# Optimization experiments

Hardware: AMD Instinct MI355X
Metric: run time of the kernel (lower is better)

The kernel has to match this reference:

```python
import jax, jax.numpy as jnp
import numpy as np

DIM, NH, HD = 1536, 12, 128
F, H, W = 1, 30, 52
SEQ = F * H * W          # 1560 tokens per AR group
NG, GI = 6, 5            # num_groups, group_idx (attend over full prefix)
POS, EPS = 1024, 1e-6


def _rope_table():
    # cos/sin table matching Wan rope_params: bands [c-2(c//3), c//3, c//3] of head_dim//2
    c = HD // 2
    parts = [c - 2 * (c // 3), c // 3, c // 3]
    pos = np.arange(POS, dtype=np.float64)
    angs = []
    for cp in parts:
        inv = 1.0 / (10000.0 ** (np.arange(cp, dtype=np.float64) / cp))
        angs.append(pos[:, None] * inv[None, :])
    ang = np.concatenate(angs, axis=1)  # [POS, c]
    return jnp.asarray(np.stack([np.cos(ang), np.sin(ang)], axis=-1), dtype=jnp.float32)


def setup_inputs() -> dict:
    key = jax.random.key(0)
    ks = jax.random.split(key, 8)
    lin = lambda k: jax.random.normal(k, (DIM, DIM), jnp.float32) * 0.02
    total = NG * SEQ
    return {
        'x': jax.random.normal(ks[0], (1, SEQ, DIM), jnp.float32),
        'wq': lin(ks[1]), 'bq': jnp.zeros((DIM,), jnp.float32),
        'wk': lin(ks[2]), 'bk': jnp.zeros((DIM,), jnp.float32),
        'wv': lin(ks[3]), 'bv': jnp.zeros((DIM,), jnp.float32),
        'wo': lin(ks[4]), 'bo': jnp.zeros((DIM,), jnp.float32),
        'nq_w': jnp.ones((DIM,), jnp.float32),
        'nk_w': jnp.ones((DIM,), jnp.float32),
        'freqs': _rope_table(),
        'k_cache': jax.random.normal(ks[5], (1, total, NH, HD), jnp.float32) * 0.5,
        'v_cache': jax.random.normal(ks[6], (1, total, NH, HD), jnp.float32) * 0.5,
        'f': F, 'h': H, 'w': W, 'group_idx': GI, 'num_groups': NG,
    }


def _rms_norm(x, weight, eps=EPS):
    # fast_rms_norm: normalize over the full channel dim, then scale
    x = x.astype(jnp.float32)
    return x * jax.lax.rsqrt(jnp.mean(x * x, axis=-1, keepdims=True) + eps) * weight


def _rope_apply(x, freqs, f, h, w, group_idx):
    # x: [B, S, N, D] with S = f*h*w; freqs: [POS, D//2, 2] (cos, sin)
    B, S, N, D = x.shape
    c = D // 2
    cf = c - 2 * (c // 3)
    ch = cw = c // 3
    sf = group_idx * f
    fp = jnp.broadcast_to(freqs[sf:sf + f, :cf][:, None, None], (f, h, w, cf, 2))
    hp = jnp.broadcast_to(freqs[:h, cf:cf + ch][None, :, None], (f, h, w, ch, 2))
    wp = jnp.broadcast_to(freqs[:w, cf + ch:][None, None, :], (f, h, w, cw, 2))
    rot = jnp.concatenate([fp, hp, wp], axis=3).reshape(S, c, 2)  # [S, c, 2]
    cos = rot[..., 0][None, :, None]  # [1, S, 1, c]
    sin = rot[..., 1][None, :, None]
    xr = x.astype(jnp.float32).reshape(B, S, N, c, 2)
    out_r = xr[..., 0] * cos - xr[..., 1] * sin  # complex multiply x * e^{i theta}
    out_i = xr[..., 0] * sin + xr[..., 1] * cos
    return jnp.stack([out_r, out_i], axis=-1).reshape(B, S, N, D)


def reference(x, wq, bq, wk, bk, wv, bv, wo, bo, nq_w, nk_w, freqs,
              k_cache, v_cache, f, h, w, group_idx, num_groups):
    B, S, C = x.shape
    n, d = NH, C // NH
    q = _rms_norm(x @ wq.T + bq, nq_w).reshape(B, S, n, d)
    k = _rms_norm(x @ wk.T + bk, nk_w).reshape(B, S, n, d)
    v = (x @ wv.T + bv).reshape(B, S, n, d)
    q = _rope_apply(q, freqs, f, h, w, group_idx)
    k = _rope_apply(k, freqs, f, h, w, group_idx)
    # KV-cache scatter (detached in the original) then prefix gather
    start = group_idx * S
    kc = jax.lax.dynamic_update_slice(k_cache, jax.lax.stop_gradient(k), (0, start, 0, 0))
    vc = jax.lax.dynamic_update_slice(v_cache, jax.lax.stop_gradient(v), (0, start, 0, 0))
    k_full = kc[:, :start + S]  # [B, Lkv, n, d]
    v_full = vc[:, :start + S]
    att = jnp.einsum('bqnd,bknd->bnqk', q, k_full) / jnp.sqrt(jnp.float32(d))
    p = jax.nn.softmax(att, axis=-1)
    o = jnp.einsum('bnqk,bknd->bqnd', p, v_full).reshape(B, S, C)
    return o @ wo.T + bo
```

## Files before the change

### kernel.cpp

```cpp
#include <hip/hip_runtime.h>

#define DIM 1536
#define NH 12
#define HD 128
#define KSPLIT 8
#define KT 32
#define MFIX 3.0f
#define KK48 48

typedef _Float16 half2_t __attribute__((ext_vector_type(2)));
typedef _Float16 half8_t __attribute__((ext_vector_type(8)));
typedef float f32x4 __attribute__((ext_vector_type(4)));

__device__ __forceinline__ half2_t pkrtz(float a, float b) {
    return __builtin_bit_cast(half2_t, __builtin_amdgcn_cvt_pkrtz(a, b));
}

__device__ __forceinline__ void split8(float4 a, float4 b, half8_t& h, half8_t& l) {
    half2_t h0 = pkrtz(a.x, a.y), h1 = pkrtz(a.z, a.w);
    half2_t h2 = pkrtz(b.x, b.y), h3 = pkrtz(b.z, b.w);
    half2_t g0 = pkrtz(a.x - (float)h0.x, a.y - (float)h0.y);
    half2_t g1 = pkrtz(a.z - (float)h1.x, a.w - (float)h1.y);
    half2_t g2 = pkrtz(b.x - (float)h2.x, b.y - (float)h2.y);
    half2_t g3 = pkrtz(b.z - (float)h3.x, b.w - (float)h3.y);
    h[0]=h0.x; h[1]=h0.y; h[2]=h1.x; h[3]=h1.y; h[4]=h2.x; h[5]=h2.y; h[6]=h3.x; h[7]=h3.y;
    l[0]=g0.x; l[1]=g0.y; l[2]=g1.x; l[3]=g1.y; l[4]=g2.x; l[5]=g2.y; l[6]=g3.x; l[7]=g3.y;
}

__device__ __forceinline__ half8_t cvt8rn(float4 a, float4 b) {
    half8_t h;
    h[0]=(_Float16)a.x; h[1]=(_Float16)a.y; h[2]=(_Float16)a.z; h[3]=(_Float16)a.w;
    h[4]=(_Float16)b.x; h[5]=(_Float16)b.y; h[6]=(_Float16)b.z; h[7]=(_Float16)b.w;
    return h;
}

__device__ __forceinline__ void gl2lds16(const void* g, void* l) {
    __builtin_amdgcn_global_load_lds(
        (const __attribute__((address_space(1))) unsigned int*)g,
        (__attribute__((address_space(3))) unsigned int*)(unsigned int)(uintptr_t)l,
        16, 0, 0);
}


__global__ __launch_bounds__(256) void cvt_a_fl(
    const float* __restrict__ src, _Float16* __restrict__ h, _Float16* __restrict__ l,
    int M, int nrec8)
{
    const int i = blockIdx.x * 256 + threadIdx.x;
    if (i >= nrec8) return;
    const int lane = i & 63;
    const int grp  = (i >> 6) & 7;
    const int tile = i >> 9;
    const int kk = tile % KK48, mt = tile / KK48;
    const int row = mt * 128 + grp * 16 + (lane & 15);
    const int k   = kk * 32 + (lane >> 4) * 8;
    float4 a = make_float4(0,0,0,0), b = a;
    if (row < M) {
        const float* s = src + (size_t)row * DIM + k;
        a = *(const float4*)s; b = *(const float4*)(s + 4);
    }
    half8_t hh, ll; split8(a, b, hh, ll);
    ((half8_t*)h)[i] = hh;
    ((half8_t*)l)[i] = ll;
}

__global__ __launch_bounds__(256) void cvt_w_fl(
    const float* __restrict__ s0, const float* __restrict__ s1,
    const float* __restrict__ s2, const float* __restrict__ s3,
    _Float16* __restrict__ h0, _Float16* __restrict__ l0,
    _Float16* __restrict__ h1, _Float16* __restrict__ l1,
    _Float16* __restrict__ h2, _Float16* __restrict__ l2,
    _Float16* __restrict__ h3, _Float16* __restrict__ l3, int nrec8)
{
    const int i = blockIdx.x * 256 + threadIdx.x;
    if (i >= nrec8) return;
    const int m = blockIdx.y;
    const float* src = m == 0 ? s0 : m == 1 ? s1 : m == 2 ? s2 : s3;
    _Float16* h = m == 0 ? h0 : m == 1 ? h1 : m == 2 ? h2 : h3;
    _Float16* l = m == 0 ? l0 : m == 1 ? l1 : m == 2 ? l2 : l3;
    const int lane = i & 63;
    const int grp  = (i >> 6) & 7;
    const int tile = i >> 9;
    const int kk = tile % KK48, nt = tile / KK48;
    const int row = nt * 128 + grp * 16 + (lane & 15);
    const int k   = kk * 32 + (lane >> 4) * 8;
    const float* s = src + (size_t)row * DIM + k;
    float4 a = *(const float4*)s, b = *(const float4*)(s + 4);
    half8_t hh, ll; split8(a, b, hh, ll);
    ((half8_t*)h)[i] = hh;
    if (m >= 2) ((half8_t*)l)[i] = ll;
}

__global__ __launch_bounds__(256, 4) void gemm_fl_s(
    const _Float16* __restrict__ Ah,
    const _Float16* __restrict__ Bh0, const _Float16* __restrict__ Bh1,
    const float* __restrict__ bias0, const float* __restrict__ bias1,
    float* __restrict__ C0, float* __restrict__ C1,
    int M)
{
    __shared__ __align__(16) _Float16 T[2][2][4096];

    const int nwg = gridDim.x;
    const int L = blockIdx.x;
    const int q8 = nwg >> 3, r8 = nwg & 7;
    const int xcd = L & 7, si = L >> 3;
    const int logical = (xcd < r8 ? xcd * (q8 + 1)
                                  : r8 * (q8 + 1) + (xcd - r8) * q8) + si;
    const int j   = logical % 24;
    const int myy = logical / 24;
    const int mat = j & 1, nt = j >> 1;
    const _Float16* Bh   = mat ? Bh1 : Bh0;
    const float*    bias = mat ? bias1 : bias0;
    float*          C    = mat ? C1 : C0;
    const int m0 = myy * 128, n0 = nt * 128;

    const int tid = threadIdx.x;
    const int lane = tid & 63, wave = tid >> 6;
    const int l16 = lane & 15, quad = lane >> 4;
    const int wm = (wave >> 1) * 64, wn = (wave & 1) * 64;

    const _Float16* Arh = Ah + (size_t)myy * KK48 * 4096;
    const _Float16* Brh = Bh + (size_t)nt  * KK48 * 4096;

    f32x4 acc[4][4];
    #pragma unroll
    for (int i = 0; i < 4; ++i)
        #pragma unroll
        for (int j2 = 0; j2 < 4; ++j2) acc[i][j2] = (f32x4){0.f, 0.f, 0.f, 0.f};

    auto STAGE = [&](int kk, int buf) {
        const size_t off = (size_t)kk * 4096 + wave * 1024 + lane * 8;
        _Float16* d0 = &T[buf][0][wave * 1024];
        _Float16* d1 = &T[buf][1][wave * 1024];
        gl2lds16(Arh + off,       d0);
        gl2lds16(Arh + off + 512, d0 + 512);
        gl2lds16(Brh + off,       d1);
        gl2lds16(Brh + off + 512, d1 + 512);
    };

    STAGE(0, 0);
    int cur = 0;
    for (int kk = 0; kk < KK48; ++kk) {
        if (kk + 1 < KK48) {
            STAGE(kk + 1, cur ^ 1);
            asm volatile("s_waitcnt vmcnt(4)" ::: "memory");
        } else {
            asm volatile("s_waitcnt vmcnt(0)" ::: "memory");
        }
        __builtin_amdgcn_s_barrier();
        __builtin_amdgcn_sched_barrier(0);

        half8_t ah[4], bh[4];
        const half8_t* tA = (const half8_t*)&T[cur][0][0];
        const half8_t* tB = (const half8_t*)&T[cur][1][0];
        #pragma unroll
        for (int ms = 0; ms < 4; ++ms) ah[ms] = tA[((wm >> 4) + ms) * 64 + lane];
        #pragma unroll
        for (int ns = 0; ns < 4; ++ns) bh[ns] = tB[((wn >> 4) + ns) * 64 + lane];

        __builtin_amdgcn_s_setprio(1);
        #pragma unroll
        for (int ms = 0; ms < 4; ++ms)
            #pragma unroll
            for (int ns = 0; ns < 4; ++ns)
                acc[ms][ns] = __builtin_amdgcn_mfma_f32_16x16x32_f16(ah[ms], bh[ns], acc[ms][ns], 0, 0, 0);
        __builtin_amdgcn_s_setprio(0);

        __builtin_amdgcn_sched_barrier(0);
        __builtin_amdgcn_s_barrier();
        cur ^= 1;
    }

    float bv[4];
    #pragma unroll
    for (int ns = 0; ns < 4; ++ns) bv[ns] = bias[n0 + wn + ns*16 + l16];
    #pragma unroll
    for (int ms = 0; ms < 4; ++ms)
        #pragma unroll
        for (int r = 0; r < 4; ++r) {
            const int row = m0 + wm + ms*16 + quad*4 + r;
            if (row < M) {
                #pragma unroll
                for (int ns = 0; ns < 4; ++ns)
                    C[(size_t)row * DIM + n0 + wn + ns*16 + l16] = acc[ms][ns][r] + bv[ns];
            }
        }
}

__global__ __launch_bounds__(256) void gemm_fl(
    const _Float16* __restrict__ Ah, const _Float16* __restrict__ Al,
    const _Float16* __restrict__ Bh, const _Float16* __restrict__ Bl,
    const float* __restrict__ bias,
    float* __restrict__ C, int M)
{
    __shared__ __align__(16) _Float16 T[2][4][4096];

    const int nwg = gridDim.x;
    const int L = blockIdx.x;
    const int q8 = nwg >> 3, r8 = nwg & 7;
    const int xcd = L & 7, si = L >> 3;
    const int logical = (xcd < r8 ? xcd * (q8 + 1)
                                  : r8 * (q8 + 1) + (xcd - r8) * q8) + si;
    const int nt  = logical % 12;
    const int myy = logical / 12;
    const int m0 = myy * 128, n0 = nt * 128;

    const int tid = threadIdx.x;
    const int lane = tid & 63, wave = tid >> 6;
    const int l16 = lane & 15, quad = lane >> 4;
    const int wm = (wave >> 1) * 64, wn = (wave & 1) * 64;

    const _Float16* Arh = Ah + (size_t)myy * KK48 * 4096;
    const _Float16* Arl = Al + (size_t)myy * KK48 * 4096;
    const _Float16* Brh = Bh + (size_t)nt  * KK48 * 4096;
    const _Float16* Brl = Bl + (size_t)nt  * KK48 * 4096;

    f32x4 acc[4][4];
    #pragma unroll
    for (int i = 0; i < 4; ++i)
        #pragma unroll
        for (int j2 = 0; j2 < 4; ++j2) acc[i][j2] = (f32x4){0.f, 0.f, 0.f, 0.f};

    auto STAGE = [&](int kk, int buf) {
        const size_t off = (size_t)kk * 4096 + wave * 1024 + lane * 8;
        _Float16* d0 = &T[buf][0][wave * 1024];
        _Float16* d1 = &T[buf][1][wave * 1024];
        _Float16* d2 = &T[buf][2][wave * 1024];
        _Float16* d3 = &T[buf][3][wave * 1024];
        gl2lds16(Arh + off,       d0);
        gl2lds16(Arh + off + 512, d0 + 512);
        gl2lds16(Arl + off,       d1);
        gl2lds16(Arl + off + 512, d1 + 512);
        gl2lds16(Brh + off,       d2);
        gl2lds16(Brh + off + 512, d2 + 512);
        gl2lds16(Brl + off,       d3);
        gl2lds16(Brl + off + 512, d3 + 512);
    };

    STAGE(0, 0);
    int cur = 0;
    for (int kk = 0; kk < KK48; ++kk) {
        if (kk + 1 < KK48) {
            STAGE(kk + 1, cur ^ 1);
            asm volatile("s_waitcnt vmcnt(8)" ::: "memory");
        } else {
            asm volatile("s_waitcnt vmcnt(0)" ::: "memory");
        }
        __builtin_amdgcn_s_barrier();
        __builtin_amdgcn_sched_barrier(0);

        half8_t ah[4], al[4], bh[4], bl[4];
        const half8_t* tA = (const half8_t*)&T[cur][0][0];
        const half8_t* tAl= (const half8_t*)&T[cur][1][0];
        const half8_t* tB = (const half8_t*)&T[cur][2][0];
        const half8_t* tBl= (const half8_t*)&T[cur][3][0];
        #pragma unroll
        for (int ms = 0; ms < 4; ++ms) {
            ah[ms] = tA [((wm >> 4) + ms) * 64 + lane];
            al[ms] = tAl[((wm >> 4) + ms) * 64 + lane];
        }
        #pragma unroll
        for (int ns = 0; ns < 4; ++ns) {
            bh[ns] = tB [((wn >> 4) + ns) * 64 + lane];
            bl[ns] = tBl[((wn >> 4) + ns) * 64 + lane];
        }
        __builtin_amdgcn_s_setprio(1);
        #pragma unroll
        for (int ms = 0; ms < 4; ++ms)
            #pragma unroll
            for (int ns = 0; ns < 4; ++ns) {
                acc[ms][ns] = __builtin_amdgcn_mfma_f32_16x16x32_f16(ah[ms], bh[ns], acc[ms][ns], 0, 0, 0);
                acc[ms][ns] = __builtin_amdgcn_mfma_f32_16x16x32_f16(ah[ms], bl[ns], acc[ms][ns], 0, 0, 0);
                acc[ms][ns] = __builtin_amdgcn_mfma_f32_16x16x32_f16(al[ms], bh[ns], acc[ms][ns], 0, 0, 0);
            }
        __builtin_amdgcn_s_setprio(0);

        __builtin_amdgcn_sched_barrier(0);
        __builtin_amdgcn_s_barrier();
        cur ^= 1;
    }

    float bv[4];
    #pragma unroll
    for (int ns = 0; ns < 4; ++ns) bv[ns] = bias[n0 + wn + ns*16 + l16];
    #pragma unroll
    for (int ms = 0; ms < 4; ++ms)
        #pragma unroll
        for (int r = 0; r < 4; ++r) {
            const int row = m0 + wm + ms*16 + quad*4 + r;
            if (row < M) {
                #pragma unroll
                for (int ns = 0; ns < 4; ++ns)
                    C[(size_t)row * DIM + n0 + wn + ns*16 + l16] = acc[ms][ns][r] + bv[ns];
            }
        }
}

__global__ __launch_bounds__(256) void rms_rope2(
    float* __restrict__ qb, float* __restrict__ kb,
    const float* __restrict__ wq_, const float* __restrict__ wk_,
    const float* __restrict__ freqs,
    const int* __restrict__ fp, const int* __restrict__ hp,
    const int* __restrict__ wp, const int* __restrict__ gip)
{
    const int s = blockIdx.x;
    float* xv = blockIdx.y ? kb : qb;
    const float* w = blockIdx.y ? wk_ : wq_;
    const int tid = threadIdx.x;
    float* row = xv + (size_t)s * DIM;
    float ss = 0.f;
    for (int c = tid; c < DIM; c += 256) { float v = row[c]; ss += v * v; }
    #pragma unroll
    for (int off = 32; off > 0; off >>= 1) ss += __shfl_down(ss, off, 64);
    __shared__ float red[4];
    if ((tid & 63) == 0) red[tid >> 6] = ss;
    __syncthreads();
    const float tot = red[0] + red[1] + red[2] + red[3];
    const float scale = rsqrtf(tot / (float)DIM + 1e-6f);
    const int f = *fp, h = *hp, ww = *wp, gi = *gip;
    const int hw = h * ww;
    const int fi = s / hw;
    const int rem = s - fi * hw;
    const int hi = rem / ww;
    const int wi = rem - hi * ww;
    const int sf = gi * f;
    for (int p = tid; p < DIM / 2; p += 256) {
        int n = p >> 6, i = p & 63;
        int pos = (i < 22) ? (sf + fi) : (i < 43) ? hi : wi;
        float cs = freqs[pos * 128 + i * 2];
        float sn = freqs[pos * 128 + i * 2 + 1];
        int base = n * HD + 2 * i;
        float x0 = row[base] * scale * w[base];
        float x1 = row[base + 1] * scale * w[base + 1];
        row[base] = x0 * cs - x1 * sn;
        row[base + 1] = x0 * sn + x1 * cs;
    }
}

__global__ __launch_bounds__(256) void kv_prep(
    const float* __restrict__ kws, const float* __restrict__ kcache,
    const float* __restrict__ vws, const float* __restrict__ vcache,
    _Float16* __restrict__ KV, int S, int NT, const int* __restrict__ gip)
{
    const int t = blockIdx.x, n = blockIdx.y;
    const int tid = threadIdx.x;
    const int lane = tid & 63;
    const int l16 = lane & 15, quad = lane >> 4;
    const int start = gip[0] * S;
    const int nk = start + S;
    _Float16* outk = KV + (size_t)(n * NT + t) * 8192;
    _Float16* outv = outk + 4096;
    #pragma unroll
    for (int fi = 0; fi < 2; ++fi) {
        const int f = (tid >> 6) + fi * 4;
        const int ks = f >> 2, db = f & 3;
        const int j = t * KT + ks * 16 + l16;
        float4 a = make_float4(0,0,0,0), b = a;
        if (j < nk) {
            const float* src = (j < start) ? (kcache + (size_t)j * DIM)
                                           : (kws + (size_t)(j - start) * DIM);
            src += n * HD + db * 32 + quad * 8;
            a = *(const float4*)src;
            b = *(const float4*)(src + 4);
        }
        *(half8_t*)&outk[(f * 64 + lane) * 8] = cvt8rn(a, b);
    }
    #pragma unroll
    for (int fi = 0; fi < 2; ++fi) {
        const int ds = (tid >> 6) + fi * 4;
        const int dim = n * HD + ds * 16 + l16;
        half8_t h;
        #pragma unroll
        for (int j = 0; j < 8; ++j) {
            const int slot = quad * 8 + j;
            const int key = t * KT + (slot >> 1) + 16 * (slot & 1);
            float v = 0.f;
            if (key < nk)
                v = (key < start) ? vcache[(size_t)key * DIM + dim]
                                  : vws[(size_t)(key - start) * DIM + dim];
            h[j] = (_Float16)v;
        }
        *(half8_t*)&outv[(ds * 64 + lane) * 8] = h;
    }
}

#define PSTRH 36
__global__ __launch_bounds__(256, 3) void attn_mfma(
    const float* __restrict__ q,
    const _Float16* __restrict__ KV,
    float* __restrict__ Op, float* __restrict__ Ml,
    int S, int NT, const int* __restrict__ gip)
{
    __shared__ __align__(16) _Float16 T[2][8192];
    __shared__ __align__(16) _Float16 Ph[4][2][16][PSTRH];

    const int nwg = gridDim.x;
    const int L = blockIdx.x;
    const int q8 = nwg >> 3, r8 = nwg & 7;
    const int xcd = L & 7, si = L >> 3;
    const int logical = (xcd < r8 ? xcd * (q8 + 1)
                                  : r8 * (q8 + 1) + (xcd - r8) * q8) + si;
    const int yb = (S + 127) >> 7;
    const int y = logical % yb;
    const int g = logical / yb;
    const int n = g % NH;
    const int ksp = g / NH;
    const int q0 = y * 128;

    const int tid = threadIdx.x;
    const int wave = tid >> 6;
    const int lane = tid & 63;
    const int l16 = lane & 15;
    const int quad = lane >> 4;
    const int start = gip[0] * S;
    const int nk = start + S;
    const int totTiles = (nk + KT - 1) / KT;
    const int tilesPer = (totTiles + KSPLIT - 1) / KSPLIT;
    const int t0 = ksp * tilesPer;
    const int t1 = min(t0 + tilesPer, totTiles);
    const float sc = 0.08838834764831845f;

    half8_t qf[2][4];
    #pragma unroll
    for (int qs = 0; qs < 2; ++qs) {
        const int qrow = q0 + wave * 32 + qs * 16 + l16;
        const bool qv = qrow < S;
        const float* qp = q + (size_t)(qv ? qrow : 0) * DIM + n * HD + quad * 8;
        #pragma unroll
        for (int db = 0; db < 4; ++db) {
            float4 a = make_float4(0,0,0,0), b = a;
            if (qv) { a = *(const float4*)(qp + db * 32); b = *(const float4*)(qp + db * 32 + 4); }
            qf[qs][db] = cvt8rn(a, b);
        }
    }

    half8_t ones_f;
    {
        _Float16 ov = (l16 == 0) ? (_Float16)1.0f : (_Float16)0.0f;
        #pragma unroll
        for (int j = 0; j < 8; ++j) ones_f[j] = ov;
    }

    f32x4 O[2][9];
    #pragma unroll
    for (int qs = 0; qs < 2; ++qs)
        #pragma unroll
        for (int ds = 0; ds < 9; ++ds) O[qs][ds] = (f32x4){0.f, 0.f, 0.f, 0.f};

    const size_t tb = (size_t)n * NT;

    if (t0 < t1) {
        const _Float16* gp = KV + (tb + t0) * 8192 + wave * 1024 + lane * 8;
        _Float16* d = &T[0][wave * 1024];
        gl2lds16(gp,              d);
        gl2lds16(gp + 512,        d + 512);
        gl2lds16(gp + 4096,       d + 4096);
        gl2lds16(gp + 4096 + 512, d + 4096 + 512);
    }

    int cur = 0;
    for (int t = t0; t < t1; ++t) {
        if (t + 1 < t1) {
            const _Float16* gp = KV + (tb + t + 1) * 8192 + wave * 1024 + lane * 8;
            _Float16* d = &T[cur ^ 1][wave * 1024];
            gl2lds16(gp,              d);
            gl2lds16(gp + 512,        d + 512);
            gl2lds16(gp + 4096,       d + 4096);
            gl2lds16(gp + 4096 + 512, d + 4096 + 512);
            asm volatile("s_waitcnt vmcnt(4)" ::: "memory");
        } else {
            asm volatile("s_waitcnt vmcnt(0)" ::: "memory");
        }
        __builtin_amdgcn_s_barrier();
        __builtin_amdgcn_sched_barrier(0);

        f32x4 sacc[2][2];
        #pragma unroll
        for (int qs = 0; qs < 2; ++qs) {
            sacc[qs][0] = (f32x4){0.f, 0.f, 0.f, 0.f};
            sacc[qs][1] = (f32x4){0.f, 0.f, 0.f, 0.f};
        }
        const half8_t* kh8 = (const half8_t*)&T[cur][0];
        __builtin_amdgcn_s_setprio(1);
        #pragma unroll
        for (int ks = 0; ks < 2; ++ks) {
            #pragma unroll
            for (int db = 0; db < 4; ++db) {
                half8_t bh = kh8[(ks * 4 + db) * 64 + lane];
                sacc[0][ks] = __builtin_amdgcn_mfma_f32_16x16x32_f16(qf[0][db], bh, sacc[0][ks], 0, 0, 0);
                sacc[1][ks] = __builtin_amdgcn_mfma_f32_16x16x32_f16(qf[1][db], bh, sacc[1][ks], 0, 0, 0);
            }
        }
        __builtin_amdgcn_s_setprio(0);

        const int k0 = t * KT;
        const bool v0 = (k0 + l16) < nk;
        const bool v1 = (k0 + 16 + l16) < nk;
        #pragma unroll
        for (int qs = 0; qs < 2; ++qs) {
            #pragma unroll
            for (int r = 0; r < 4; ++r) {
                float p0 = v0 ? __expf(sacc[qs][0][r] * sc - MFIX) : 0.f;
                float p1 = v1 ? __expf(sacc[qs][1][r] * sc - MFIX) : 0.f;
                half2_t pp;
                pp.x = (_Float16)p0;
                pp.y = (_Float16)p1;
                *(half2_t*)&Ph[wave][qs][quad * 4 + r][2 * l16] = pp;
            }
        }

        half8_t ph[2];
        #pragma unroll
        for (int qs = 0; qs < 2; ++qs)
            ph[qs] = *(const half8_t*)&Ph[wave][qs][l16][quad * 8];

        const half8_t* vt8 = (const half8_t*)&T[cur][4096];
        __builtin_amdgcn_s_setprio(1);
        #pragma unroll
        for (int ds = 0; ds < 8; ++ds) {
            half8_t vh = vt8[ds * 64 + lane];
            O[0][ds] = __builtin_amdgcn_mfma_f32_16x16x32_f16(ph[0], vh, O[0][ds], 0, 0, 0);
            O[1][ds] = __builtin_amdgcn_mfma_f32_16x16x32_f16(ph[1], vh, O[1][ds], 0, 0, 0);
        }
        O[0][8] = __builtin_amdgcn_mfma_f32_16x16x32_f16(ph[0], ones_f, O[0][8], 0, 0, 0);
        O[1][8] = __builtin_amdgcn_mfma_f32_16x16x32_f16(ph[1], ones_f, O[1][8], 0, 0, 0);
        __builtin_amdgcn_s_setprio(0);

        __builtin_amdgcn_sched_barrier(0);
        __builtin_amdgcn_s_barrier();
        cur ^= 1;
    }

    #pragma unroll
    for (int qs = 0; qs < 2; ++qs)
        #pragma unroll
        for (int r = 0; r < 4; ++r) {
            const int row = q0 + wave * 32 + qs * 16 + quad * 4 + r;
            if (row < S) {
                float* op = Op + (((size_t)ksp * NH + n) * S + row) * HD + l16;
                #pragma unroll
                for (int ds = 0; ds < 8; ++ds) op[ds * 16] = O[qs][ds][r];
                if (l16 == 0)
                    Ml[((size_t)ksp * NH + n) * S + row] = O[qs][8][r];
            }
        }
}

__global__ __launch_bounds__(256) void attn_merge(
    const float* __restrict__ Op, const float* __restrict__ Ml,
    _Float16* __restrict__ oh, _Float16* __restrict__ ol, int S)
{
    const int idx = blockIdx.x * 256 + threadIdx.x;
    const int total = NH * S * HD / 2;
    if (idx >= total) return;
    const int d0 = (idx & 63) * 2;
    const int t = idx >> 6;
    const int row = t % S;
    const int n = t / S;
    float num0 = 0.f, num1 = 0.f, den = 0.f;
    #pragma unroll
    for (int ks = 0; ks < KSPLIT; ++ks) {
        const size_t base = ((size_t)ks * NH + n) * S + row;
        num0 += Op[base * HD + d0];
        num1 += Op[base * HD + d0 + 1];
        den += Ml[base];
    }
    const float v0 = num0 / den, v1 = num1 / den;
    half2_t h = pkrtz(v0, v1);
    half2_t l = pkrtz(v0 - (float)h.x, v1 - (float)h.y);
    const int k = n * HD + d0;
    const int mt = row >> 7, rr = row & 127;
    const int grp = rr >> 4, l16r = rr & 15;
    const int kk = k >> 5, quad = (k & 31) >> 3, jj = k & 7;
    const size_t a = ((size_t)(mt * KK48 + kk) * 4096)
                   + ((size_t)(grp * 64 + quad * 16 + l16r) * 8) + jj;
    *(half2_t*)&oh[a] = h;
    *(half2_t*)&ol[a] = l;
}

extern "C" void kernel_launch(void* const* d_in, const int* in_sizes, int n_in,
                              void* d_out, int out_size, void* d_ws, size_t ws_size,
                              hipStream_t stream)
{
    const float* x      = (const float*)d_in[0];
    const float* wq     = (const float*)d_in[1];
    const float* bq     = (const float*)d_in[2];
    const float* wk     = (const float*)d_in[3];
    const float* bk     = (const float*)d_in[4];
    const float* wv     = (const float*)d_in[5];
    const float* bv     = (const float*)d_in[6];
    const float* wo     = (const float*)d_in[7];
    const float* bo     = (const float*)d_in[8];
    const float* nqw    = (const float*)d_in[9];
    const float* nkw    = (const float*)d_in[10];
    const float* freqs  = (const float*)d_in[11];
    const float* kcache = (const float*)d_in[12];
    const float* vcache = (const float*)d_in[13];
    const int*   fp     = (const int*)d_in[14];
    const int*   hp     = (const int*)d_in[15];
    const int*   wp     = (const int*)d_in[16];
    const int*   gip    = (const int*)d_in[17];

    const int S = in_sizes[0] / DIM;
    const int total = in_sizes[12] / (NH * HD);
    const int NT = (total + KT - 1) / KT;
    const int MT = (S + 127) / 128;
    const size_t sd = (size_t)S * DIM;
    const size_t arec = (size_t)MT * KK48 * 4096;
    const size_t wrec = (size_t)12 * KK48 * 4096;

    char* p = (char*)d_ws;
    float* q  = (float*)p;            p += sd * 4;
    float* k  = (float*)p;            p += sd * 4;
    float* v  = (float*)p;            p += sd * 4;
    float* Op = (float*)p;            p += (size_t)KSPLIT * NH * S * HD * 4;
    float* Ml = (float*)p;            p += (size_t)KSPLIT * NH * S * 4;
    _Float16* KV  = (_Float16*)p;     p += (size_t)NH * NT * 8192 * 2;
    _Float16* xh  = (_Float16*)p;     p += arec * 2;
    _Float16* xl  = (_Float16*)p;     p += arec * 2;
    _Float16* oh  = (_Float16*)p;     p += arec * 2;
    _Float16* ol  = (_Float16*)p;     p += arec * 2;
    _Float16* wqh = (_Float16*)p;     p += wrec * 2;
    _Float16* wql = (_Float16*)p;     p += wrec * 2;
    _Float16* wkh = (_Float16*)p;     p += wrec * 2;
    _Float16* wkl = (_Float16*)p;     p += wrec * 2;
    _Float16* wvh = (_Float16*)p;     p += wrec * 2;
    _Float16* wvl = (_Float16*)p;     p += wrec * 2;
    _Float16* woh = (_Float16*)p;     p += wrec * 2;
    _Float16* wol = (_Float16*)p;     p += wrec * 2;
    float* out = (float*)d_out;

    const int an8 = (int)(arec / 8), wn8 = (int)(wrec / 8);

    cvt_a_fl<<<dim3((an8 + 255) / 256), dim3(256), 0, stream>>>(x, xh, xl, S, an8);
    cvt_w_fl<<<dim3((wn8 + 255) / 256, 4), dim3(256), 0, stream>>>(
        wq, wk, wv, wo, wqh, wql, wkh, wkl, wvh, wvl, woh, wol, wn8);

    gemm_fl_s<<<dim3(24 * MT), dim3(256), 0, stream>>>(
        xh, wqh, wkh, bq, bk, q, k, S);
    gemm_fl<<<dim3(12 * MT), dim3(256), 0, stream>>>(
        xh, xl, wvh, wvl, bv, v, S);
    rms_rope2<<<dim3(S, 2), dim3(256), 0, stream>>>(q, k, nqw, nkw, freqs, fp, hp, wp, gip);
    kv_prep<<<dim3(NT, NH), dim3(256), 0, stream>>>(k, kcache, v, vcache, KV, S, NT, gip);
    {
        const int yb = (S + 127) / 128;
        const int nwg = NH * yb * KSPLIT;
        attn_mfma<<<dim3(nwg), dim3(256), 0, stream>>>(
            q, KV, Op, Ml, S, NT, gip);
    }
    attn_merge<<<dim3((NH * S * HD / 2 + 255) / 256), dim3(256), 0, stream>>>(Op, Ml, oh, ol, S);
    gemm_fl<<<dim3(12 * MT), dim3(256), 0, stream>>>(
        oh, ol, woh, wol, bo, out, S);
}
```

Measured before the change: 459.9 us.

## Fuse fp32-to-fp16 activation conversion into QKV GEMMs and vectorize V packing

Drops the separate cvt_a_fl kernel and the xh/xl workspace. The QK and V GEMMs now read fp32 x directly into registers, convert it (hi only, or a hi/lo split for V) and write the tiles into LDS, with the load for the next k-step overlapping the MFMAs. The V half of kv_prep switches from strided scalar gathers to row-wise float4 loads with scattered fp16 stores. In exchange, each GEMM block reads twice as many bytes of A per tile and does the conversion work repeatedly across the N tiles, and the new register-staged A path adds a vmcnt(0) wait inside the loop.

```diff
diff --git a/kernel.cpp b/kernel.cpp
--- a/kernel.cpp
+++ b/kernel.cpp
@@ -27,6 +27,14 @@
     l[0]=g0.x; l[1]=g0.y; l[2]=g1.x; l[3]=g1.y; l[4]=g2.x; l[5]=g2.y; l[6]=g3.x; l[7]=g3.y;
 }
 
+__device__ __forceinline__ half8_t hi8(float4 a, float4 b) {
+    half2_t h0 = pkrtz(a.x, a.y), h1 = pkrtz(a.z, a.w);
+    half2_t h2 = pkrtz(b.x, b.y), h3 = pkrtz(b.z, b.w);
+    half8_t h;
+    h[0]=h0.x; h[1]=h0.y; h[2]=h1.x; h[3]=h1.y; h[4]=h2.x; h[5]=h2.y; h[6]=h3.x; h[7]=h3.y;
+    return h;
+}
+
 __device__ __forceinline__ half8_t cvt8rn(float4 a, float4 b) {
     half8_t h;
     h[0]=(_Float16)a.x; h[1]=(_Float16)a.y; h[2]=(_Float16)a.z; h[3]=(_Float16)a.w;
@@ -41,28 +49,6 @@
         16, 0, 0);
 }
 
-
-__global__ __launch_bounds__(256) void cvt_a_fl(
-    const float* __restrict__ src, _Float16* __restrict__ h, _Float16* __restrict__ l,
-    int M, int nrec8)
-{
-    const int i = blockIdx.x * 256 + threadIdx.x;
-    if (i >= nrec8) return;
-    const int lane = i & 63;
-    const int grp  = (i >> 6) & 7;
-    const int tile = i >> 9;
-    const int kk = tile % KK48, mt = tile / KK48;
-    const int row = mt * 128 + grp * 16 + (lane & 15);
-    const int k   = kk * 32 + (lane >> 4) * 8;
-    float4 a = make_float4(0,0,0,0), b = a;
-    if (row < M) {
-        const float* s = src + (size_t)row * DIM + k;
-        a = *(const float4*)s; b = *(const float4*)(s + 4);
-    }
-    half8_t hh, ll; split8(a, b, hh, ll);
-    ((half8_t*)h)[i] = hh;
-    ((half8_t*)l)[i] = ll;
-}
 
 __global__ __launch_bounds__(256) void cvt_w_fl(
     const float* __restrict__ s0, const float* __restrict__ s1,
@@ -92,7 +78,7 @@
 }
 
 __global__ __launch_bounds__(256, 4) void gemm_fl_s(
-    const _Float16* __restrict__ Ah,
+    const float* __restrict__ X,
     const _Float16* __restrict__ Bh0, const _Float16* __restrict__ Bh1,
     const float* __restrict__ bias0, const float* __restrict__ bias1,
     float* __restrict__ C0, float* __restrict__ C1,
@@ -119,8 +105,16 @@
     const int l16 = lane & 15, quad = lane >> 4;
     const int wm = (wave >> 1) * 64, wn = (wave & 1) * 64;
 
-    const _Float16* Arh = Ah + (size_t)myy * KK48 * 4096;
-    const _Float16* Brh = Bh + (size_t)nt  * KK48 * 4096;
+    const int i0 = tid * 2;
+    const int g0 = i0 >> 6,     lr0 = i0 & 63;
+    const int g1 = (i0+1) >> 6, lr1 = (i0+1) & 63;
+    const int row0 = m0 + g0 * 16 + (lr0 & 15);
+    const int row1 = m0 + g1 * 16 + (lr1 & 15);
+    const bool r0v = row0 < M, r1v = row1 < M;
+    const float* x0 = X + (size_t)(r0v ? row0 : 0) * DIM + (lr0 >> 4) * 8;
+    const float* x1 = X + (size_t)(r1v ? row1 : 0) * DIM + (lr1 >> 4) * 8;
+
+    const _Float16* Brh = Bh + (size_t)nt * KK48 * 4096;
 
     f32x4 acc[4][4];
     #pragma unroll
@@ -128,26 +122,35 @@
         #pragma unroll
         for (int j2 = 0; j2 < 4; ++j2) acc[i][j2] = (f32x4){0.f, 0.f, 0.f, 0.f};
 
-    auto STAGE = [&](int kk, int buf) {
+    float4 a0, a1, a2, a3;
+    auto LOADA = [&](int kk) {
+        float4 z = make_float4(0,0,0,0);
+        a0 = a1 = a2 = a3 = z;
+        if (r0v) { a0 = *(const float4*)(x0 + kk*32); a1 = *(const float4*)(x0 + kk*32 + 4); }
+        if (r1v) { a2 = *(const float4*)(x1 + kk*32); a3 = *(const float4*)(x1 + kk*32 + 4); }
+    };
+    auto STAGEB = [&](int kk, int buf) {
         const size_t off = (size_t)kk * 4096 + wave * 1024 + lane * 8;
-        _Float16* d0 = &T[buf][0][wave * 1024];
-        _Float16* d1 = &T[buf][1][wave * 1024];
-        gl2lds16(Arh + off,       d0);
-        gl2lds16(Arh + off + 512, d0 + 512);
-        gl2lds16(Brh + off,       d1);
-        gl2lds16(Brh + off + 512, d1 + 512);
+        _Float16* d = &T[buf][1][wave * 1024];
+        gl2lds16(Brh + off,       d);
+        gl2lds16(Brh + off + 512, d + 512);
     };
-
-    STAGE(0, 0);
+    auto WRITEA = [&](int buf) {
+        *(half8_t*)&T[buf][0][(size_t)i0 * 8]       = hi8(a0, a1);
+        *(half8_t*)&T[buf][0][(size_t)(i0 + 1) * 8] = hi8(a2, a3);
+    };
+
+    LOADA(0); STAGEB(0, 0);
+    asm volatile("s_waitcnt vmcnt(0)" ::: "memory");
+    WRITEA(0);
+    asm volatile("s_waitcnt lgkmcnt(0)" ::: "memory");
+    __builtin_amdgcn_s_barrier();
+
     int cur = 0;
     for (int kk = 0; kk < KK48; ++kk) {
-        if (kk + 1 < KK48) {
-            STAGE(kk + 1, cur ^ 1);
-            asm volatile("s_waitcnt vmcnt(4)" ::: "memory");
-        } else {
-            asm volatile("s_waitcnt vmcnt(0)" ::: "memory");
-        }
-        __builtin_amdgcn_s_barrier();
+        __builtin_amdgcn_sched_barrier(0);
+        const bool more = (kk + 1 < KK48);
+        if (more) { LOADA(kk + 1); STAGEB(kk + 1, cur ^ 1); }
         __builtin_amdgcn_sched_barrier(0);
 
         half8_t ah[4], bh[4];
@@ -166,6 +169,143 @@
                 acc[ms][ns] = __builtin_amdgcn_mfma_f32_16x16x32_f16(ah[ms], bh[ns], acc[ms][ns], 0, 0, 0);
         __builtin_amdgcn_s_setprio(0);
 
+        if (more) {
+            asm volatile("s_waitcnt vmcnt(0)" ::: "memory");
+            WRITEA(cur ^ 1);
+        }
+        asm volatile("s_waitcnt lgkmcnt(0)" ::: "memory");
+        __builtin_amdgcn_sched_barrier(0);
+        __builtin_amdgcn_s_barrier();
+        cur ^= 1;
+    }
+
+    float bv[4];
+    #pragma unroll
+    for (int ns = 0; ns < 4; ++ns) bv[ns] = bias[n0 + wn + ns*16 + l16];
+    #pragma unroll
+    for (int ms = 0; ms < 4; ++ms)
+        #pragma unroll
+        for (int r = 0; r < 4; ++r) {
+            const int row = m0 + wm + ms*16 + quad*4 + r;
+            if (row < M) {
+                #pragma unroll
+                for (int ns = 0; ns < 4; ++ns)
+                    C[(size_t)row * DIM + n0 + wn + ns*16 + l16] = acc[ms][ns][r] + bv[ns];
+            }
+        }
+}
+
+__global__ __launch_bounds__(256) void gemm_fl_d(
+    const float* __restrict__ X,
+    const _Float16* __restrict__ Bh, const _Float16* __restrict__ Bl,
+    const float* __restrict__ bias,
+    float* __restrict__ C, int M)
+{
+    __shared__ __align__(16) _Float16 T[2][4][4096];
+
+    const int nwg = gridDim.x;
+    const int L = blockIdx.x;
+    const int q8 = nwg >> 3, r8 = nwg & 7;
+    const int xcd = L & 7, si = L >> 3;
+    const int logical = (xcd < r8 ? xcd * (q8 + 1)
+                                  : r8 * (q8 + 1) + (xcd - r8) * q8) + si;
+    const int nt  = logical % 12;
+    const int myy = logical / 12;
+    const int m0 = myy * 128, n0 = nt * 128;
+
+    const int tid = threadIdx.x;
+    const int lane = tid & 63, wave = tid >> 6;
+    const int l16 = lane & 15, quad = lane >> 4;
+    const int wm = (wave >> 1) * 64, wn = (wave & 1) * 64;
+
+    const int i0 = tid * 2;
+    const int g0 = i0 >> 6,     lr0 = i0 & 63;
+    const int g1 = (i0+1) >> 6, lr1 = (i0+1) & 63;
+    const int row0 = m0 + g0 * 16 + (lr0 & 15);
+    const int row1 = m0 + g1 * 16 + (lr1 & 15);
+    const bool r0v = row0 < M, r1v = row1 < M;
+    const float* x0 = X + (size_t)(r0v ? row0 : 0) * DIM + (lr0 >> 4) * 8;
+    const float* x1 = X + (size_t)(r1v ? row1 : 0) * DIM + (lr1 >> 4) * 8;
+
+    const _Float16* Brh = Bh + (size_t)nt * KK48 * 4096;
+    const _Float16* Brl = Bl + (size_t)nt * KK48 * 4096;
+
+    f32x4 acc[4][4];
+    #pragma unroll
+    for (int i = 0; i < 4; ++i)
+        #pragma unroll
+        for (int j2 = 0; j2 < 4; ++j2) acc[i][j2] = (f32x4){0.f, 0.f, 0.f, 0.f};
+
+    float4 a0, a1, a2, a3;
+    auto LOADA = [&](int kk) {
+        float4 z = make_float4(0,0,0,0);
+        a0 = a1 = a2 = a3 = z;
+        if (r0v) { a0 = *(const float4*)(x0 + kk*32); a1 = *(const float4*)(x0 + kk*32 + 4); }
+        if (r1v) { a2 = *(const float4*)(x1 + kk*32); a3 = *(const float4*)(x1 + kk*32 + 4); }
+    };
+    auto STAGEB = [&](int kk, int buf) {
+        const size_t off = (size_t)kk * 4096 + wave * 1024 + lane * 8;
+        _Float16* d2 = &T[buf][2][wave * 1024];
+        _Float16* d3 = &T[buf][3][wave * 1024];
+        gl2lds16(Brh + off,       d2);
+        gl2lds16(Brh + off + 512, d2 + 512);
+        gl2lds16(Brl + off,       d3);
+        gl2lds16(Brl + off + 512, d3 + 512);
+    };
+    auto WRITEA = [&](int buf) {
+        half8_t h, l;
+        split8(a0, a1, h, l);
+        *(half8_t*)&T[buf][0][(size_t)i0 * 8] = h;
+        *(half8_t*)&T[buf][1][(size_t)i0 * 8] = l;
+        split8(a2, a3, h, l);
+        *(half8_t*)&T[buf][0][(size_t)(i0 + 1) * 8] = h;
+        *(half8_t*)&T[buf][1][(size_t)(i0 + 1) * 8] = l;
+    };
+
+    LOADA(0); STAGEB(0, 0);
+    asm volatile("s_waitcnt vmcnt(0)" ::: "memory");
+    WRITEA(0);
+    asm volatile("s_waitcnt lgkmcnt(0)" ::: "memory");
+    __builtin_amdgcn_s_barrier();
+
+    int cur = 0;
+    for (int kk = 0; kk < KK48; ++kk) {
+        __builtin_amdgcn_sched_barrier(0);
+        const bool more = (kk + 1 < KK48);
+        if (more) { LOADA(kk + 1); STAGEB(kk + 1, cur ^ 1); }
+        __builtin_amdgcn_sched_barrier(0);
+
+        half8_t ah[4], al[4], bh[4], bl[4];
+        const half8_t* tA = (const half8_t*)&T[cur][0][0];
+        const half8_t* tAl= (const half8_t*)&T[cur][1][0];
+        const half8_t* tB = (const half8_t*)&T[cur][2][0];
+        const half8_t* tBl= (const half8_t*)&T[cur][3][0];
+        #pragma unroll
+        for (int ms = 0; ms < 4; ++ms) {
+            ah[ms] = tA [((wm >> 4) + ms) * 64 + lane];
+            al[ms] = tAl[((wm >> 4) + ms) * 64 + lane];
+        }
+        #pragma unroll
+        for (int ns = 0; ns < 4; ++ns) {
+            bh[ns] = tB [((wn >> 4) + ns) * 64 + lane];
+            bl[ns] = tBl[((wn >> 4) + ns) * 64 + lane];
+        }
+        __builtin_amdgcn_s_setprio(1);
+        #pragma unroll
+        for (int ms = 0; ms < 4; ++ms)
+            #pragma unroll
+            for (int ns = 0; ns < 4; ++ns) {
+                acc[ms][ns] = __builtin_amdgcn_mfma_f32_16x16x32_f16(ah[ms], bh[ns], acc[ms][ns], 0, 0, 0);
+                acc[ms][ns] = __builtin_amdgcn_mfma_f32_16x16x32_f16(ah[ms], bl[ns], acc[ms][ns], 0, 0, 0);
+                acc[ms][ns] = __builtin_amdgcn_mfma_f32_16x16x32_f16(al[ms], bh[ns], acc[ms][ns], 0, 0, 0);
+            }
+        __builtin_amdgcn_s_setprio(0);
+
+        if (more) {
+            asm volatile("s_waitcnt vmcnt(0)" ::: "memory");
+            WRITEA(cur ^ 1);
+        }
+        asm volatile("s_waitcnt lgkmcnt(0)" ::: "memory");
         __builtin_amdgcn_sched_barrier(0);
         __builtin_amdgcn_s_barrier();
         cur ^= 1;
@@ -365,22 +505,30 @@
         }
         *(half8_t*)&outk[(f * 64 + lane) * 8] = cvt8rn(a, b);
     }
-    #pragma unroll
-    for (int fi = 0; fi < 2; ++fi) {
-        const int ds = (tid >> 6) + fi * 4;
-        const int dim = n * HD + ds * 16 + l16;
-        half8_t h;
-        #pragma unroll
-        for (int j = 0; j < 8; ++j) {
-            const int slot = quad * 8 + j;
-            const int key = t * KT + (slot >> 1) + 16 * (slot & 1);
-            float v = 0.f;
-            if (key < nk)
-                v = (key < start) ? vcache[(size_t)key * DIM + dim]
-                                  : vws[(size_t)(key - start) * DIM + dim];
-            h[j] = (_Float16)v;
-        }
-        *(half8_t*)&outv[(ds * 64 + lane) * 8] = h;
+    {
+        const int r  = tid >> 3;
+        const int c0 = (tid & 7) * 16;
+        const int key = t * KT + r;
+        const int s  = (r & 15) * 2 + (r >> 4);
+        float4 va = make_float4(0,0,0,0), vb = va, vc = va, vd = va;
+        if (key < nk) {
+            const float* src = (key < start) ? (vcache + (size_t)key * DIM)
+                                             : (vws + (size_t)(key - start) * DIM);
+            src += n * HD + c0;
+            va = ((const float4*)src)[0];
+            vb = ((const float4*)src)[1];
+            vc = ((const float4*)src)[2];
+            vd = ((const float4*)src)[3];
+        }
+        _Float16* o = outv + ((size_t)((c0 >> 4) * 64 + (s >> 3) * 16) * 8) + (s & 7);
+        o[0]   = (_Float16)va.x; o[8]   = (_Float16)va.y;
+        o[16]  = (_Float16)va.z; o[24]  = (_Float16)va.w;
+        o[32]  = (_Float16)vb.x; o[40]  = (_Float16)vb.y;
+        o[48]  = (_Float16)vb.z; o[56]  = (_Float16)vb.w;
+        o[64]  = (_Float16)vc.x; o[72]  = (_Float16)vc.y;
+        o[80]  = (_Float16)vc.z; o[88]  = (_Float16)vc.w;
+        o[96]  = (_Float16)vd.x; o[104] = (_Float16)vd.y;
+        o[112] = (_Float16)vd.z; o[120] = (_Float16)vd.w;
     }
 }
 
@@ -616,8 +764,6 @@
     float* Op = (float*)p;            p += (size_t)KSPLIT * NH * S * HD * 4;
     float* Ml = (float*)p;            p += (size_t)KSPLIT * NH * S * 4;
     _Float16* KV  = (_Float16*)p;     p += (size_t)NH * NT * 8192 * 2;
-    _Float16* xh  = (_Float16*)p;     p += arec * 2;
-    _Float16* xl  = (_Float16*)p;     p += arec * 2;
     _Float16* oh  = (_Float16*)p;     p += arec * 2;
     _Float16* ol  = (_Float16*)p;     p += arec * 2;
     _Float16* wqh = (_Float16*)p;     p += wrec * 2;
@@ -630,16 +776,15 @@
     _Float16* wol = (_Float16*)p;     p += wrec * 2;
     float* out = (float*)d_out;
 
-    const int an8 = (int)(arec / 8), wn8 = (int)(wrec / 8);
-
-    cvt_a_fl<<<dim3((an8 + 255) / 256), dim3(256), 0, stream>>>(x, xh, xl, S, an8);
+    const int wn8 = (int)(wrec / 8);
+
     cvt_w_fl<<<dim3((wn8 + 255) / 256, 4), dim3(256), 0, stream>>>(
         wq, wk, wv, wo, wqh, wql, wkh, wkl, wvh, wvl, woh, wol, wn8);
 
     gemm_fl_s<<<dim3(24 * MT), dim3(256), 0, stream>>>(
-        xh, wqh, wkh, bq, bk, q, k, S);
-    gemm_fl<<<dim3(12 * MT), dim3(256), 0, stream>>>(
-        xh, xl, wvh, wvl, bv, v, S);
+        x, wqh, wkh, bq, bk, q, k, S);
+    gemm_fl_d<<<dim3(12 * MT), dim3(256), 0, stream>>>(
+        x, wvh, wvl, bv, v, S);
     rms_rope2<<<dim3(S, 2), dim3(256), 0, stream>>>(q, k, nqw, nkw, freqs, fp, hp, wp, gip);
     kv_prep<<<dim3(NT, NH), dim3(256), 0, stream>>>(k, kcache, v, vcache, KV, S, NT, gip);
     {
```

Measured after the change: 507.3 us. 10.3% more time.
